# Kernel tuning notes

Hardware: AMD Instinct MI355X
Metric: run time of the kernel (lower is better)

Reference implementation:

```python
import jax, jax.numpy as jnp
import numpy as np

B, S, D_IN, D_OUT, H = 4, 2048, 2048, 2048, 16
HD = D_OUT // H  # head_dim = 128


def setup_inputs() -> dict:
    key = jax.random.key(0)
    ks = jax.random.split(key, 5)
    s = 0.02
    return {
        "x": jax.random.normal(ks[0], (B, S, D_IN), dtype=jnp.float32),
        "W_q": jax.random.normal(ks[1], (D_IN, D_OUT), dtype=jnp.float32) * s,
        "W_k": jax.random.normal(ks[2], (D_IN, D_OUT), dtype=jnp.float32) * s,
        "W_v": jax.random.normal(ks[3], (D_IN, D_OUT), dtype=jnp.float32) * s,
        "W_o": jax.random.normal(ks[4], (D_OUT, D_OUT), dtype=jnp.float32) * s,
        "b_o": jnp.zeros((D_OUT,), dtype=jnp.float32),
    }


def reference(x, W_q, W_k, W_v, W_o, b_o):
    b, n, _ = x.shape
    # projections (qkv_bias=False), split into heads: [b, h, n, hd]
    q = (x @ W_q).reshape(b, n, H, HD).transpose(0, 2, 1, 3)
    k = (x @ W_k).reshape(b, n, H, HD).transpose(0, 2, 1, 3)
    v = (x @ W_v).reshape(b, n, H, HD).transpose(0, 2, 1, 3)
    # scores [b, h, n, n], causal mask (triu, diagonal=1) applied BEFORE scaling
    scores = jnp.einsum("bhqd,bhkd->bhqk", q, k)
    causal = jnp.triu(jnp.ones((n, n), dtype=bool), k=1)
    scores = jnp.where(causal, -jnp.inf, scores)
    scale = jnp.asarray(HD, scores.dtype) ** 0.5
    attn = jax.nn.softmax(scores / scale, axis=-1)
    ctx = jnp.einsum("bhqk,bhkd->bhqd", attn, v)
    ctx = ctx.transpose(0, 2, 1, 3).reshape(b, n, D_OUT)
    return ctx @ W_o + b_o
```

## Files before the change

kernel.cpp:

```cpp
#include <hip/hip_runtime.h>
#include <hip/hip_bf16.h>
#include <math.h>

#define H_   16
#define S_   2048
#define D_   2048
#define HD_  128
#define B_   4
#define M_   8192

typedef __attribute__((ext_vector_type(8))) short short8;
typedef __attribute__((ext_vector_type(4))) short short4v;
typedef __attribute__((ext_vector_type(4))) float f32x4;

__device__ __forceinline__ short f2bf(float f) {
  unsigned u = __float_as_uint(f);
  u += 0x7fff + ((u >> 16) & 1);
  return (short)(u >> 16);
}

__device__ __forceinline__ unsigned pk2(float a, float b) {
  __hip_bfloat162 h = __float22bfloat162_rn(float2{a, b});
  union { __hip_bfloat162 h2; unsigned u; } c;
  c.h2 = h;
  return c.u;
}

__device__ __forceinline__ void async16(const void* g, void* l) {
  __builtin_amdgcn_global_load_lds(
      (const __attribute__((address_space(1))) void*)g,
      (__attribute__((address_space(3))) void*)l, 16, 0, 0);
}

__global__ void k_cvtx(const float* __restrict__ x, short* __restrict__ o, int n4) {
  const int i = blockIdx.x * 256 + threadIdx.x;
  if (i >= n4) return;
  const float4 f = ((const float4*)x)[i];
  short4v s;
  s.x = f2bf(f.x); s.y = f2bf(f.y); s.z = f2bf(f.z); s.w = f2bf(f.w);
  ((short4v*)o)[i] = s;
}

__global__ void k_wtrans4(const float* __restrict__ W0, const float* __restrict__ W1,
                          const float* __restrict__ W2, const float* __restrict__ W3,
                          short* __restrict__ T0, short* __restrict__ T1,
                          short* __restrict__ T2, short* __restrict__ T3) {
  __shared__ float t[32][33];
  const int z = blockIdx.z;
  const float* W = z == 0 ? W0 : z == 1 ? W1 : z == 2 ? W2 : W3;
  short* Wt      = z == 0 ? T0 : z == 1 ? T1 : z == 2 ? T2 : T3;
  const int n0 = blockIdx.x << 5, k0 = blockIdx.y << 5;
  const int tc = threadIdx.x & 31, tr = threadIdx.x >> 5;
#pragma unroll
  for (int i = 0; i < 32; i += 8)
    t[tr + i][tc] = W[(size_t)(k0 + tr + i) * D_ + n0 + tc];
  __syncthreads();
#pragma unroll
  for (int i = 0; i < 32; i += 8)
    Wt[(size_t)(n0 + tr + i) * D_ + k0 + tc] = f2bf(t[tc][tr + i]);
}


#define GBAR() asm volatile("s_barrier" ::: "memory")
#define WLG0()                                          \
  do {                                                  \
    asm volatile("s_waitcnt lgkmcnt(0)" ::: "memory");  \
    __builtin_amdgcn_sched_barrier(0);                  \
  } while (0)

#define STG_A(b, mh, t)                                           \
  do {                                                            \
    const size_t o_ = (size_t)(t) * 64 + (size_t)(mh) * 64 * K;   \
    async16(Ag0 + o_, &As[b][mh][ldst]);                          \
    async16(Ag1 + o_, &As[b][mh][4096 + ldst]);                   \
  } while (0)

#define STG_B(b, nh, t)                                           \
  do {                                                            \
    const size_t o_ = (size_t)(t) * 64 + (size_t)(nh) * 32 * K;   \
    async16(Bg0 + o_, &Bs[b][nh][ldst]);                          \
    async16(Bg1 + o_, &Bs[b][nh][4096 + ldst]);                   \
  } while (0)

#define LDS_A(b, mh)                                                     \
  do {                                                                   \
    const char* a_ = (const char*)&As[b][mh][0];                         \
    _Pragma("unroll") for (int mi_ = 0; mi_ < 4; ++mi_) {                \
      af[mi_ * 2]     = *(const short8*)(a_ + rdA + mi_ * 2048 + cc0);   \
      af[mi_ * 2 + 1] = *(const short8*)(a_ + rdA + mi_ * 2048 + cc1);   \
    }                                                                    \
  } while (0)

#define LDS_B(b, nh, BF)                                                 \
  do {                                                                   \
    const char* b_ = (const char*)&Bs[b][nh][0];                         \
    _Pragma("unroll") for (int ni_ = 0; ni_ < 2; ++ni_) {                \
      BF[ni_ * 2]     = *(const short8*)(b_ + rdB + ni_ * 2048 + cc0);   \
      BF[ni_ * 2 + 1] = *(const short8*)(b_ + rdB + ni_ * 2048 + cc1);   \
    }                                                                    \
  } while (0)

#define QUAD(mh, nh, BF)                                                   \
  do {                                                                     \
    __builtin_amdgcn_s_setprio(1);                                         \
    _Pragma("unroll") for (int mi_ = 0; mi_ < 4; ++mi_)                    \
    _Pragma("unroll") for (int ni_ = 0; ni_ < 2; ++ni_) {                  \
      acc[(mh) * 4 + mi_][(nh) * 2 + ni_] =                                \
          __builtin_amdgcn_mfma_f32_16x16x32_bf16(                         \
              af[mi_ * 2], BF[ni_ * 2],                                    \
              acc[(mh) * 4 + mi_][(nh) * 2 + ni_], 0, 0, 0);               \
      acc[(mh) * 4 + mi_][(nh) * 2 + ni_] =                                \
          __builtin_amdgcn_mfma_f32_16x16x32_bf16(                         \
              af[mi_ * 2 + 1], BF[ni_ * 2 + 1],                            \
              acc[(mh) * 4 + mi_][(nh) * 2 + ni_], 0, 0, 0);               \
    }                                                                      \
    __builtin_amdgcn_s_setprio(0);                                         \
  } while (0)

#define TILE(T, b)                                                  \
  do {                                                              \
                           \
    LDS_A(b, 0);                                                    \
    LDS_B(b, 0, bf0);                                               \
    if ((T) + 1 < NT) STG_A((b) ^ 1, 1, (T) + 1);                   \
    asm volatile("s_waitcnt lgkmcnt(8)" ::: "memory");              \
    GBAR();                                                         \
    WLG0();                                                         \
    QUAD(0, 0, bf0);                                                \
    GBAR();                                                         \
                           \
    LDS_B(b, 1, bf1);                                               \
    if ((T) + 2 < NT) STG_A(b, 0, (T) + 2);                         \
    GBAR();                                                         \
    WLG0();                                                         \
    QUAD(0, 1, bf1);                                                \
    GBAR();                                                         \
                           \
    LDS_A(b, 1);                                                    \
    if ((T) + 2 < NT) STG_B(b, 0, (T) + 2);                         \
    GBAR();                                                         \
    WLG0();                                                         \
    QUAD(1, 0, bf0);                                                \
    GBAR();                                                         \
                           \
    if ((T) + 2 < NT) STG_B(b, 1, (T) + 2);                         \
    if ((T) + 2 < NT)                                               \
      asm volatile("s_waitcnt vmcnt(6)" ::: "memory");              \
    else if ((T) + 1 < NT)                                          \
      asm volatile("s_waitcnt vmcnt(0)" ::: "memory");              \
    GBAR();                                                         \
    QUAD(1, 1, bf1);                                                \
    GBAR();                                                         \
  } while (0)

template <int MODE>
__global__ __launch_bounds__(512, 2)
void k_gemm256(const short* __restrict__ A, const short* __restrict__ Bt,
               void* __restrict__ C0, void* __restrict__ C1, void* __restrict__ C2,
               const float* __restrict__ bias, int M, int N, int K) {
  __shared__ __align__(16) short As[2][2][8192];
  __shared__ __align__(16) short Bs[2][2][8192];
  const int tid = threadIdx.x;
  const int lane = tid & 63;
  const int wave = tid >> 6;
  const int ln = lane & 15, lq = lane >> 4;
  const int wr = wave >> 2, wc = wave & 3;

  const int gx = (MODE == 0) ? 24 : 8;
  const int nwg = (MODE == 0) ? 768 : 256;
  const int w = blockIdx.y * gx + blockIdx.x;
  const int lg = (w & 7) * (nwg >> 3) + (w >> 3);
  const int bn = (lg % gx) << 8;
  const int bm = (lg / gx) << 8;
  const int NT = K >> 6;

  const int r0 = wave * 8 + (lane >> 3);
  const int k0 = ((lane & 7) ^ ((lane >> 3) & 7)) << 3;
  const short* Ag0 = A  + (size_t)(bm + r0) * K + k0;
  const short* Ag1 = A  + (size_t)(bm + 128 + r0) * K + k0;
  const short* Bg0 = Bt + (size_t)(bn + ((r0 >> 5) << 6) + (r0 & 31)) * K + k0;
  const short* Bg1 = Bt + (size_t)(bn + (((r0 >> 5) + 2) << 6) + (r0 & 31)) * K + k0;
  const int ldst = wave * 512;

  const int swz = (ln & 7) << 4;
  const int rdA = (wr * 64 + ln) * 128;
  const int rdB = (wc * 32 + ln) * 128;
  const int cc0 = (lq * 16) ^ swz;
  const int cc1 = (64 + lq * 16) ^ swz;

  f32x4 acc[8][4];
#pragma unroll
  for (int i = 0; i < 8; i++)
#pragma unroll
    for (int j = 0; j < 4; j++) acc[i][j] = (f32x4)0.0f;

  STG_A(0, 0, 0);
  STG_B(0, 0, 0);
  STG_B(0, 1, 0);
  STG_A(0, 1, 0);
  asm volatile("s_waitcnt vmcnt(4)" ::: "memory");
  STG_A(1, 0, 1);
  STG_B(1, 0, 1);
  STG_B(1, 1, 1);
  asm volatile("s_waitcnt vmcnt(6)" ::: "memory");
  GBAR();

  short8 af[8];
  short8 bf0[4], bf1[4];

#pragma unroll 1
  for (int T = 0; T < NT; T += 2) {
    TILE(T, 0);
    TILE(T + 1, 1);
  }

  if (MODE == 0) {
    const int proj = bn >> 11;
    const int cb = bn & 2047;
    if (proj < 2) {
      short* C = (short*)(proj == 0 ? C0 : C1);
#pragma unroll
      for (int mi = 0; mi < 8; mi++)
#pragma unroll
        for (int ni = 0; ni < 4; ni++) {
          const int col = cb + wc * 64 + ni * 16 + ln;
          const int h = col >> 7, d = col & 127;
#pragma unroll
          for (int r = 0; r < 4; r++) {
            const int row = bm + wr * 128 + mi * 16 + lq * 4 + r;
            const int bb = row >> 11, s = row & 2047;
            C[((size_t)((bb * H_ + h) * S_ + s)) * HD_ + d] = f2bf(acc[mi][ni][r]);
          }
        }
    } else {
      short* C = (short*)C2;
#pragma unroll
      for (int mi = 0; mi < 8; mi++)
#pragma unroll
        for (int ni = 0; ni < 4; ni++) {
          const int col = cb + wc * 64 + ni * 16 + ln;
          const int h = col >> 7, d = col & 127;
          const int row0 = bm + wr * 128 + mi * 16 + lq * 4;
          const int bb = row0 >> 11, s = row0 & 2047;
          short4v pk;
#pragma unroll
          for (int r = 0; r < 4; r++) pk[r] = f2bf(acc[mi][ni][r]);
          *(short4v*)(C + ((size_t)((bb * H_ + h) * HD_ + d)) * S_ + s) = pk;
        }
    }
  } else {
    float* C = (float*)C0;
#pragma unroll
    for (int mi = 0; mi < 8; mi++)
#pragma unroll
      for (int ni = 0; ni < 4; ni++) {
        const int col = bn + wc * 64 + ni * 16 + ln;
        const float bv = bias[col];
#pragma unroll
        for (int r = 0; r < 4; r++) {
          const int row = bm + wr * 128 + mi * 16 + lq * 4 + r;
          C[(size_t)row * N + col] = acc[mi][ni][r] + bv;
        }
      }
  }
}

__global__ __launch_bounds__(512)
void k_flash(const short* __restrict__ Q, const short* __restrict__ K,
             const short* __restrict__ Vt, short* __restrict__ ctx) {
  __shared__ __align__(16) short Ks[2][64 * 128];
  __shared__ __align__(16) short Vs[2][128 * 64];
  __shared__ __align__(16) short Ps[8 * 32 * 64];

  const int tid = threadIdx.x, lane = tid & 63, w = tid >> 6;
  const int ln = lane & 15, lq = lane >> 4;
  const int bx = blockIdx.x;
  const int bh = ((bx & 7) << 3) | ((bx >> 3) & 7);
  const int cpair = bx >> 6;
  const int b = bh >> 4, h = bh & 15;
  const short* Qp = Q  + (size_t)bh * S_ * HD_;
  const short* Kp = K  + (size_t)bh * S_ * HD_;
  const short* Vp = Vt + (size_t)bh * HD_ * S_;

  const float sc = 0.08838834764831845f * 1.4426950408889634f;
  const int lx = ln & 7;

  int koff[2], voff[2];
#pragma unroll
  for (int it = 0; it < 2; it++) {
    const int kr = w * 8 + it * 4 + (lane >> 4);
    koff[it] = kr * HD_ + (((lane & 15) ^ (kr & 7)) * 8);
    const int vr = w * 16 + it * 8 + (lane >> 3);
    voff[it] = vr * S_ + (((lane & 7) ^ (vr & 7)) * 8);
  }

#pragma unroll 1
  for (int pass = 0; pass < 2; pass++) {
    const int chunk = pass ? (7 - cpair) : cpair;
    const int q0 = chunk << 8;
    const int qw = q0 + w * 32;
    const int nkt = chunk * 4 + 4;

    short8 qf[2][4];
#pragma unroll
    for (int nt = 0; nt < 2; nt++)
#pragma unroll
      for (int c = 0; c < 4; c++)
        qf[nt][c] = *(const short8*)(Qp + (size_t)(qw + nt * 16 + ln) * HD_ + c * 32 + lq * 8);

    f32x4 acc[8][2];
#pragma unroll
    for (int t = 0; t < 8; t++) { acc[t][0] = (f32x4)0.0f; acc[t][1] = (f32x4)0.0f; }
    float l_i[2] = {0.0f, 0.0f};

    __syncthreads();
#pragma unroll
    for (int it = 0; it < 2; it++) {
      async16(Kp + koff[it], &Ks[0][(w * 8 + it * 4) * 128]);
      async16(Vp + voff[it], &Vs[0][(w * 16 + it * 8) * 64]);
    }

#pragma unroll 1
    for (int kt = 0; kt < nkt; kt++) {
      const int k0 = kt << 6;
      const int cur = kt & 1;
      __syncthreads();
      if (kt + 1 < nkt) {
        const int nk0 = (kt + 1) << 6;
        const int nb = cur ^ 1;
#pragma unroll
        for (int it = 0; it < 2; it++) {
          async16(Kp + (size_t)nk0 * HD_ + koff[it], &Ks[nb][(w * 8 + it * 4) * 128]);
          async16(Vp + nk0 + voff[it],               &Vs[nb][(w * 16 + it * 8) * 64]);
        }
      }

      if (k0 <= qw + 31) {
        const short* KsC = Ks[cur];
        const short* VsC = Vs[cur];
        short* Pw = Ps + w * 32 * 64;
        const bool dg = (k0 + 63 > qw);

#pragma unroll
        for (int mt = 0; mt < 4; mt++) {
          f32x4 s0 = (f32x4)0.0f, s1 = (f32x4)0.0f;
          __builtin_amdgcn_s_setprio(1);
#pragma unroll
          for (int c = 0; c < 4; c++) {
            short8 kf = *(const short8*)(KsC + (mt * 16 + ln) * 128 + (((4 * c + lq) ^ lx) * 8));
            s0 = __builtin_amdgcn_mfma_f32_16x16x32_bf16(kf, qf[0][c], s0, 0, 0, 0);
            s1 = __builtin_amdgcn_mfma_f32_16x16x32_bf16(kf, qf[1][c], s1, 0, 0, 0);
          }
          __builtin_amdgcn_s_setprio(0);
          if (dg) {
#pragma unroll
            for (int r = 0; r < 4; r++) {
              const int kv = k0 + mt * 16 + lq * 4 + r;
              if (kv > qw + ln)      s0[r] = -INFINITY; else s0[r] *= sc;
              if (kv > qw + 16 + ln) s1[r] = -INFINITY; else s1[r] *= sc;
            }
          } else {
#pragma unroll
            for (int r = 0; r < 4; r++) { s0[r] *= sc; s1[r] *= sc; }
          }
#pragma unroll
          for (int r = 0; r < 4; r++) {
            s0[r] = exp2f(s0[r]); l_i[0] += s0[r];
            s1[r] = exp2f(s1[r]); l_i[1] += s1[r];
          }
          const int swc = (2 * mt + (lq >> 1)) ^ lx;
          const int po = swc * 8 + (lq & 1) * 4;
          *(uint2*)(Pw + ln * 64 + po)        = uint2{pk2(s0[0], s0[1]), pk2(s0[2], s0[3])};
          *(uint2*)(Pw + (16 + ln) * 64 + po) = uint2{pk2(s1[0], s1[1]), pk2(s1[2], s1[3])};
        }
        __asm__ volatile("s_waitcnt lgkmcnt(0)" ::: "memory");

#pragma unroll
        for (int c = 0; c < 2; c++) {
          const int swr = ((4 * c + lq) ^ lx) * 8;
          short8 pf0 = *(const short8*)(Pw + ln * 64 + swr);
          short8 pf1 = *(const short8*)(Pw + (16 + ln) * 64 + swr);
          __builtin_amdgcn_s_setprio(1);
#pragma unroll
          for (int t = 0; t < 8; t++) {
            short8 vf = *(const short8*)(VsC + (t * 16 + ln) * 64 + swr);
            acc[t][0] = __builtin_amdgcn_mfma_f32_16x16x32_bf16(vf, pf0, acc[t][0], 0, 0, 0);
            acc[t][1] = __builtin_amdgcn_mfma_f32_16x16x32_bf16(vf, pf1, acc[t][1], 0, 0, 0);
          }
          __builtin_amdgcn_s_setprio(0);
        }
      }
    }

#pragma unroll
    for (int o = 16; o < 64; o <<= 1) {
      l_i[0] += __shfl_xor(l_i[0], o, 64);
      l_i[1] += __shfl_xor(l_i[1], o, 64);
    }
    const float il[2] = {1.0f / l_i[0], 1.0f / l_i[1]};

#pragma unroll
    for (int t = 0; t < 8; t++)
#pragma unroll
      for (int nt = 0; nt < 2; nt++) {
        const int q = qw + nt * 16 + ln;
        const int d = t * 16 + lq * 4;
        uint2 o2 = {pk2(acc[t][nt][0] * il[nt], acc[t][nt][1] * il[nt]),
                    pk2(acc[t][nt][2] * il[nt], acc[t][nt][3] * il[nt])};
        *(uint2*)(ctx + ((size_t)(b * S_ + q)) * D_ + h * HD_ + d) = o2;
      }
  }
}

extern "C" void kernel_launch(void* const* d_in, const int* in_sizes, int n_in,
                              void* d_out, int out_size, void* d_ws, size_t ws_size,
                              hipStream_t stream) {
  const float* x  = (const float*)d_in[0];
  const float* Wq = (const float*)d_in[1];
  const float* Wk = (const float*)d_in[2];
  const float* Wv = (const float*)d_in[3];
  const float* Wo = (const float*)d_in[4];
  const float* bo = (const float*)d_in[5];
  float* out = (float*)d_out;

  char* ws = (char*)d_ws;
  const size_t SZ_X = (size_t)M_ * D_ * sizeof(short);
  const size_t SZ_W = (size_t)D_ * D_ * sizeof(short);
  short* xb  = (short*)(ws);
  short* Wqt = (short*)(ws + SZ_X);
  short* Wkt = (short*)(ws + SZ_X + SZ_W);
  short* Wvt = (short*)(ws + SZ_X + 2 * SZ_W);
  short* Wot = (short*)(ws + SZ_X + 3 * SZ_W);
  short* Qb  = (short*)(ws + SZ_X + 4 * SZ_W);
  short* Kb  = (short*)(ws + 2 * SZ_X + 4 * SZ_W);
  short* Vtb = (short*)(ws + 3 * SZ_X + 4 * SZ_W);
  short* ctx = (short*)(ws + 4 * SZ_X + 4 * SZ_W);

  k_cvtx<<<M_ * D_ / 4 / 256, 256, 0, stream>>>(x, xb, M_ * D_ / 4);
  dim3 tg(D_ / 32, D_ / 32, 4);
  k_wtrans4<<<tg, 256, 0, stream>>>(Wq, Wk, Wv, Wo, Wqt, Wkt, Wvt, Wot);

  dim3 gq(3 * D_ / 256, M_ / 256);
  k_gemm256<0><<<gq, 512, 0, stream>>>(xb, Wqt, Qb, Kb, Vtb, nullptr, M_, 3 * D_, D_);

  k_flash<<<256, 512, 0, stream>>>(Qb, Kb, Vtb, ctx);

  dim3 go(D_ / 256, M_ / 256);
  k_gemm256<1><<<go, 512, 0, stream>>>(ctx, Wot, out, nullptr, nullptr, bo, M_, D_, D_);
}
```

Before: 550.1 us.

## Make QKV GEMM persistent with next-tile prefetch overlapping epilogue; merge prep kernels

Merges the x conversion and the weight transpose into a single prep launch, using an extra z-slice of the grid for the x conversion. The QKV GEMM now launches 256 persistent workgroups, each handling three output tiles, and issues the global-to-LDS loads for the next tile before running the current tile's epilogue stores, so stores overlap with loads. The output GEMM launches 256 blocks with one tile each. The prologue wait is simplified to a full vmcnt(0), which may lose some overlap in the initial staging.

```diff
diff --git a/kernel.cpp b/kernel.cpp
--- a/kernel.cpp
+++ b/kernel.cpp
@@ -32,21 +32,25 @@
       (__attribute__((address_space(3))) void*)l, 16, 0, 0);
 }
 
-__global__ void k_cvtx(const float* __restrict__ x, short* __restrict__ o, int n4) {
-  const int i = blockIdx.x * 256 + threadIdx.x;
-  if (i >= n4) return;
-  const float4 f = ((const float4*)x)[i];
-  short4v s;
-  s.x = f2bf(f.x); s.y = f2bf(f.y); s.z = f2bf(f.z); s.w = f2bf(f.w);
-  ((short4v*)o)[i] = s;
-}
-
-__global__ void k_wtrans4(const float* __restrict__ W0, const float* __restrict__ W1,
-                          const float* __restrict__ W2, const float* __restrict__ W3,
-                          short* __restrict__ T0, short* __restrict__ T1,
-                          short* __restrict__ T2, short* __restrict__ T3) {
+__global__ void k_prep(const float* __restrict__ W0, const float* __restrict__ W1,
+                       const float* __restrict__ W2, const float* __restrict__ W3,
+                       short* __restrict__ T0, short* __restrict__ T1,
+                       short* __restrict__ T2, short* __restrict__ T3,
+                       const float* __restrict__ x, short* __restrict__ xb) {
+  const int z = blockIdx.z;
+  if (z == 4) {
+    const int base = (blockIdx.y * 64 + blockIdx.x) * 256 + threadIdx.x;
+#pragma unroll
+    for (int j = 0; j < 4; ++j) {
+      const int i = base + j * 1048576;
+      const float4 f = ((const float4*)x)[i];
+      short4v s;
+      s.x = f2bf(f.x); s.y = f2bf(f.y); s.z = f2bf(f.z); s.w = f2bf(f.w);
+      ((short4v*)xb)[i] = s;
+    }
+    return;
+  }
   __shared__ float t[32][33];
-  const int z = blockIdx.z;
   const float* W = z == 0 ? W0 : z == 1 ? W1 : z == 2 ? W2 : W3;
   short* Wt      = z == 0 ? T0 : z == 1 ? T1 : z == 2 ? T2 : T3;
   const int n0 = blockIdx.x << 5, k0 = blockIdx.y << 5;
@@ -80,6 +84,17 @@
     const size_t o_ = (size_t)(t) * 64 + (size_t)(nh) * 32 * K;   \
     async16(Bg0 + o_, &Bs[b][nh][ldst]);                          \
     async16(Bg1 + o_, &Bs[b][nh][4096 + ldst]);                   \
+  } while (0)
+
+#define STAGE7()    \
+  do {              \
+    STG_A(0, 0, 0); \
+    STG_B(0, 0, 0); \
+    STG_B(0, 1, 0); \
+    STG_A(0, 1, 0); \
+    STG_A(1, 0, 1); \
+    STG_B(1, 0, 1); \
+    STG_B(1, 1, 1); \
   } while (0)
 
 #define LDS_A(b, mh)                                                     \
@@ -165,21 +180,14 @@
   const int wave = tid >> 6;
   const int ln = lane & 15, lq = lane >> 4;
   const int wr = wave >> 2, wc = wave & 3;
-
-  const int gx = (MODE == 0) ? 24 : 8;
-  const int nwg = (MODE == 0) ? 768 : 256;
-  const int w = blockIdx.y * gx + blockIdx.x;
-  const int lg = (w & 7) * (nwg >> 3) + (w >> 3);
-  const int bn = (lg % gx) << 8;
-  const int bm = (lg / gx) << 8;
   const int NT = K >> 6;
+
+  constexpr int TPB = (MODE == 0) ? 3 : 1;
+  constexpr int gx  = (MODE == 0) ? 24 : 8;
+  constexpr int nwg = (MODE == 0) ? 768 : 256;
 
   const int r0 = wave * 8 + (lane >> 3);
   const int k0 = ((lane & 7) ^ ((lane >> 3) & 7)) << 3;
-  const short* Ag0 = A  + (size_t)(bm + r0) * K + k0;
-  const short* Ag1 = A  + (size_t)(bm + 128 + r0) * K + k0;
-  const short* Bg0 = Bt + (size_t)(bn + ((r0 >> 5) << 6) + (r0 & 31)) * K + k0;
-  const short* Bg1 = Bt + (size_t)(bn + (((r0 >> 5) + 2) << 6) + (r0 & 31)) * K + k0;
   const int ldst = wave * 512;
 
   const int swz = (ln & 7) << 4;
@@ -188,80 +196,110 @@
   const int cc0 = (lq * 16) ^ swz;
   const int cc1 = (64 + lq * 16) ^ swz;
 
+  int wg = blockIdx.x;
+  int lg = (wg & 7) * (nwg >> 3) + (wg >> 3);
+  int bn = (lg % gx) << 8;
+  int bm = (lg / gx) << 8;
+
+  const short* Ag0 = A  + (size_t)(bm + r0) * K + k0;
+  const short* Ag1 = A  + (size_t)(bm + 128 + r0) * K + k0;
+  const short* Bg0 = Bt + (size_t)(bn + ((r0 >> 5) << 6) + (r0 & 31)) * K + k0;
+  const short* Bg1 = Bt + (size_t)(bn + (((r0 >> 5) + 2) << 6) + (r0 & 31)) * K + k0;
+
   f32x4 acc[8][4];
 #pragma unroll
   for (int i = 0; i < 8; i++)
 #pragma unroll
     for (int j = 0; j < 4; j++) acc[i][j] = (f32x4)0.0f;
 
-  STG_A(0, 0, 0);
-  STG_B(0, 0, 0);
-  STG_B(0, 1, 0);
-  STG_A(0, 1, 0);
-  asm volatile("s_waitcnt vmcnt(4)" ::: "memory");
-  STG_A(1, 0, 1);
-  STG_B(1, 0, 1);
-  STG_B(1, 1, 1);
-  asm volatile("s_waitcnt vmcnt(6)" ::: "memory");
+  STAGE7();
+  asm volatile("s_waitcnt vmcnt(0)" ::: "memory");
   GBAR();
 
   short8 af[8];
   short8 bf0[4], bf1[4];
 
 #pragma unroll 1
-  for (int T = 0; T < NT; T += 2) {
-    TILE(T, 0);
-    TILE(T + 1, 1);
-  }
-
-  if (MODE == 0) {
-    const int proj = bn >> 11;
-    const int cb = bn & 2047;
-    if (proj < 2) {
-      short* C = (short*)(proj == 0 ? C0 : C1);
+  for (int ti = 0; ti < TPB; ++ti) {
+#pragma unroll 1
+    for (int T = 0; T < NT; T += 2) {
+      TILE(T, 0);
+      TILE(T + 1, 1);
+    }
+
+    int nbn = 0, nbm = 0;
+    if (ti + 1 < TPB) {
+      const int nwg_id = blockIdx.x + (ti + 1) * 256;
+      const int nlg = (nwg_id & 7) * (nwg >> 3) + (nwg_id >> 3);
+      nbn = (nlg % gx) << 8;
+      nbm = (nlg / gx) << 8;
+      Ag0 = A  + (size_t)(nbm + r0) * K + k0;
+      Ag1 = A  + (size_t)(nbm + 128 + r0) * K + k0;
+      Bg0 = Bt + (size_t)(nbn + ((r0 >> 5) << 6) + (r0 & 31)) * K + k0;
+      Bg1 = Bt + (size_t)(nbn + (((r0 >> 5) + 2) << 6) + (r0 & 31)) * K + k0;
+      STAGE7();
+    }
+
+    if (MODE == 0) {
+      const int proj = bn >> 11;
+      const int cb = bn & 2047;
+      if (proj < 2) {
+        short* C = (short*)(proj == 0 ? C0 : C1);
+#pragma unroll
+        for (int mi = 0; mi < 8; mi++)
+#pragma unroll
+          for (int ni = 0; ni < 4; ni++) {
+            const int col = cb + wc * 64 + ni * 16 + ln;
+            const int h = col >> 7, d = col & 127;
+#pragma unroll
+            for (int r = 0; r < 4; r++) {
+              const int row = bm + wr * 128 + mi * 16 + lq * 4 + r;
+              const int bb = row >> 11, s = row & 2047;
+              C[((size_t)((bb * H_ + h) * S_ + s)) * HD_ + d] = f2bf(acc[mi][ni][r]);
+            }
+          }
+      } else {
+        short* C = (short*)C2;
+#pragma unroll
+        for (int mi = 0; mi < 8; mi++)
+#pragma unroll
+          for (int ni = 0; ni < 4; ni++) {
+            const int col = cb + wc * 64 + ni * 16 + ln;
+            const int h = col >> 7, d = col & 127;
+            const int row0 = bm + wr * 128 + mi * 16 + lq * 4;
+            const int bb = row0 >> 11, s = row0 & 2047;
+            short4v pk;
+#pragma unroll
+            for (int r = 0; r < 4; r++) pk[r] = f2bf(acc[mi][ni][r]);
+            *(short4v*)(C + ((size_t)((bb * H_ + h) * HD_ + d)) * S_ + s) = pk;
+          }
+      }
+    } else {
+      float* C = (float*)C0;
 #pragma unroll
       for (int mi = 0; mi < 8; mi++)
 #pragma unroll
         for (int ni = 0; ni < 4; ni++) {
-          const int col = cb + wc * 64 + ni * 16 + ln;
-          const int h = col >> 7, d = col & 127;
+          const int col = bn + wc * 64 + ni * 16 + ln;
+          const float bv = bias[col];
 #pragma unroll
           for (int r = 0; r < 4; r++) {
             const int row = bm + wr * 128 + mi * 16 + lq * 4 + r;
-            const int bb = row >> 11, s = row & 2047;
-            C[((size_t)((bb * H_ + h) * S_ + s)) * HD_ + d] = f2bf(acc[mi][ni][r]);
+            C[(size_t)row * N + col] = acc[mi][ni][r] + bv;
           }
         }
-    } else {
-      short* C = (short*)C2;
-#pragma unroll
-      for (int mi = 0; mi < 8; mi++)
-#pragma unroll
-        for (int ni = 0; ni < 4; ni++) {
-          const int col = cb + wc * 64 + ni * 16 + ln;
-          const int h = col >> 7, d = col & 127;
-          const int row0 = bm + wr * 128 + mi * 16 + lq * 4;
-          const int bb = row0 >> 11, s = row0 & 2047;
-          short4v pk;
-#pragma unroll
-          for (int r = 0; r < 4; r++) pk[r] = f2bf(acc[mi][ni][r]);
-          *(short4v*)(C + ((size_t)((bb * H_ + h) * HD_ + d)) * S_ + s) = pk;
-        }
-    }
-  } else {
-    float* C = (float*)C0;
-#pragma unroll
-    for (int mi = 0; mi < 8; mi++)
-#pragma unroll
-      for (int ni = 0; ni < 4; ni++) {
-        const int col = bn + wc * 64 + ni * 16 + ln;
-        const float bv = bias[col];
-#pragma unroll
-        for (int r = 0; r < 4; r++) {
-          const int row = bm + wr * 128 + mi * 16 + lq * 4 + r;
-          C[(size_t)row * N + col] = acc[mi][ni][r] + bv;
-        }
-      }
+    }
+
+    if (ti + 1 < TPB) {
+      asm volatile("s_waitcnt vmcnt(0)" ::: "memory");
+      GBAR();
+      bn = nbn;
+      bm = nbm;
+#pragma unroll
+      for (int i = 0; i < 8; i++)
+#pragma unroll
+        for (int j = 0; j < 4; j++) acc[i][j] = (f32x4)0.0f;
+    }
   }
 }
 
@@ -436,15 +474,12 @@
   short* Vtb = (short*)(ws + 3 * SZ_X + 4 * SZ_W);
   short* ctx = (short*)(ws + 4 * SZ_X + 4 * SZ_W);
 
-  k_cvtx<<<M_ * D_ / 4 / 256, 256, 0, stream>>>(x, xb, M_ * D_ / 4);
-  dim3 tg(D_ / 32, D_ / 32, 4);
-  k_wtrans4<<<tg, 256, 0, stream>>>(Wq, Wk, Wv, Wo, Wqt, Wkt, Wvt, Wot);
-
-  dim3 gq(3 * D_ / 256, M_ / 256);
-  k_gemm256<0><<<gq, 512, 0, stream>>>(xb, Wqt, Qb, Kb, Vtb, nullptr, M_, 3 * D_, D_);
+  dim3 tg(D_ / 32, D_ / 32, 5);
+  k_prep<<<tg, 256, 0, stream>>>(Wq, Wk, Wv, Wo, Wqt, Wkt, Wvt, Wot, x, xb);
+
+  k_gemm256<0><<<256, 512, 0, stream>>>(xb, Wqt, Qb, Kb, Vtb, nullptr, M_, 3 * D_, D_);
 
   k_flash<<<256, 512, 0, stream>>>(Qb, Kb, Vtb, ctx);
 
-  dim3 go(D_ / 256, M_ / 256);
-  k_gemm256<1><<<go, 512, 0, stream>>>(ctx, Wot, out, nullptr, nullptr, bo, M_, D_, D_);
-}
+  k_gemm256<1><<<256, 512, 0, stream>>>(ctx, Wot, out, nullptr, nullptr, bo, M_, D_, D_);
+}
```

Result: no change. 554.3 us (+0.8%).
